# Kernel tuning notes

Hardware: AMD Instinct MI355X
Metric: run time of the kernel (lower is better)

## Reference

```python
import jax, jax.numpy as jnp
import numpy as np

H = 1024        # hidden_size
M = 1024        # memory_size
NH = 16         # num_heads
DH = H // NH    # head_dim
CR = 4          # compression_ratio
B, S = 4, 2048


def _lin(x, W, b):
    return x @ W + b


def setup_inputs() -> dict:
    key = jax.random.key(0)
    ks = iter(jax.random.split(key, 32))
    p = lambda *shape: jax.random.normal(next(ks), shape, dtype=jnp.float32) * 0.02
    inp = {
        'hidden_states': jax.random.normal(next(ks), (B, S, H), dtype=jnp.float32),
        'memory_bank': jax.random.normal(next(ks), (B, M, H), dtype=jnp.float32),
        'memory_mask': jnp.ones((B, M), dtype=bool),
        'write_pointer': 700,
        # compressor: Linear(H*CR -> H), SiLU, Linear(H -> H)
        'Wc1': p(H * CR, H), 'bc1': jnp.zeros((H,), jnp.float32),
        'Wc2': p(H, H), 'bc2': jnp.zeros((H,), jnp.float32),
        # attention projections
        'Wq': p(H, H), 'bq': jnp.zeros((H,), jnp.float32),
        'Wk': p(H, H), 'bk': jnp.zeros((H,), jnp.float32),
        'Wv': p(H, H), 'bv': jnp.zeros((H,), jnp.float32),
        'Wo': p(H, H), 'bo': jnp.zeros((H,), jnp.float32),
        # write gate: Linear(H -> H//2), SiLU, Linear(H//2 -> 1), Sigmoid
        'Wwg1': p(H, H // 2), 'bwg1': jnp.zeros((H // 2,), jnp.float32),
        'Wwg2': p(H // 2, 1), 'bwg2': jnp.zeros((1,), jnp.float32),
        # read gate: Linear(2H -> H//2), SiLU, Linear(H//2 -> 1), Sigmoid
        'Wrg1': p(2 * H, H // 2), 'brg1': jnp.zeros((H // 2,), jnp.float32),
        'Wrg2': p(H // 2, 1), 'brg2': jnp.zeros((1,), jnp.float32),
        # LayerNorm
        'ln_g': jnp.ones((H,), jnp.float32), 'ln_b': jnp.zeros((H,), jnp.float32),
    }
    return inp


def _forward(hidden_states, memory_bank, memory_mask, write_pointer,
             Wc1, bc1, Wc2, bc2, Wq, bq, Wk, bk, Wv, bv, Wo, bo,
             Wwg1, bwg1, Wwg2, bwg2, Wrg1, brg1, Wrg2, brg2, ln_g, ln_b):
    # ---- memory attention ----
    q = _lin(hidden_states, Wq, bq).reshape(B, S, NH, DH)
    k = _lin(memory_bank, Wk, bk).reshape(B, M, NH, DH)
    v = _lin(memory_bank, Wv, bv).reshape(B, M, NH, DH)
    scale = DH ** -0.5
    scores = jnp.einsum('bqhd,bkhd->bhqk', q, k) * scale
    scores = jnp.where(memory_mask[:, None, None, :], scores, -jnp.inf)
    probs = jnp.nan_to_num(jax.nn.softmax(scores, axis=-1), nan=0.0)
    retrieved = jnp.einsum('bhqk,bkhd->bqhd', probs, v).reshape(B, S, H)
    retrieved = _lin(retrieved, Wo, bo)

    # ---- read gate + residual + layernorm ----
    gate_in = jnp.concatenate([hidden_states, retrieved], axis=-1)
    rg = jax.nn.sigmoid(_lin(jax.nn.silu(_lin(gate_in, Wrg1, brg1)), Wrg2, brg2))
    out = hidden_states + rg * retrieved
    mu = jnp.mean(out, axis=-1, keepdims=True)
    var = jnp.var(out, axis=-1, keepdims=True)
    out = (out - mu) * jax.lax.rsqrt(var + 1e-5) * ln_g + ln_b

    # ---- write to memory ----
    wg = jax.nn.sigmoid(_lin(jax.nn.silu(_lin(hidden_states, Wwg1, bwg1)), Wwg2, bwg2))  # [B,S,1]
    L = S // CR  # S divisible by CR -> no padding needed (pad path is a no-op)
    compressed = _lin(jax.nn.silu(_lin(hidden_states.reshape(B, L, CR * H), Wc1, bc1)), Wc2, bc2)
    wg = wg.reshape(B, L, CR, 1).mean(axis=2)
    gated = compressed * wg  # [B,L,H]

    idx = (write_pointer + jnp.arange(L)) % M  # circular-buffer indices (unique since L <= M)
    new_bank = memory_bank.at[:, idx].set(gated)
    new_mask = memory_mask.at[:, idx].set(True)
    new_ptr = (write_pointer + L) % M
    return out, new_bank, new_mask, new_ptr


def reference(hidden_states, memory_bank, memory_mask, write_pointer,
              Wc1, bc1, Wc2, bc2, Wq, bq, Wk, bk, Wv, bv, Wo, bo,
              Wwg1, bwg1, Wwg2, bwg2, Wrg1, brg1, Wrg2, brg2, ln_g, ln_b):
    return _forward(hidden_states, memory_bank, memory_mask, write_pointer,
                    Wc1, bc1, Wc2, bc2, Wq, bq, Wk, bk, Wv, bv, Wo, bo,
                    Wwg1, bwg1, Wwg2, bwg2, Wrg1, brg1, Wrg2, brg2, ln_g, ln_b)
```

## Files before the change

### kernel.cpp

```cpp
#include <hip/hip_runtime.h>
#include <hip/hip_bf16.h>

#define Bb 4
#define Ss 2048
#define Hh 1024
#define Mm 1024
#define NHh 16
#define DHh 64
#define CRr 4
#define Ll (Ss / CRr)

typedef __attribute__((ext_vector_type(8))) short short8;
typedef __attribute__((ext_vector_type(4))) float f32x4;
typedef __attribute__((ext_vector_type(16))) float f32x16;

typedef __attribute__((address_space(1))) const unsigned int g_u32;
typedef __attribute__((address_space(3))) unsigned int l_u32;

__device__ inline void gload_lds16(const void* g, void* l) {
    __builtin_amdgcn_global_load_lds((g_u32*)g, (l_u32*)l, 16, 0, 0);
}

__device__ inline unsigned short f2bf(float x) {
    unsigned int u = __builtin_bit_cast(unsigned int, x);
    unsigned int r = u + 0x7FFFu + ((u >> 16) & 1u);
    return (unsigned short)(r >> 16);
}
__device__ inline float bf2f(unsigned short u) {
    return __builtin_bit_cast(float, (unsigned int)u << 16);
}
__device__ inline unsigned int cvtpk_bf16(float lo, float hi2) {
    unsigned int r;
    asm("v_cvt_pk_bf16_f32 %0, %1, %2" : "=v"(r) : "v"(lo), "v"(hi2));
    return r;
}
__device__ inline f32x16 zero16() {
    f32x16 v;
    #pragma unroll
    for (int i = 0; i < 16; ++i) v[i] = 0.0f;
    return v;
}
__device__ inline short8 lds_frag(const unsigned short* base, int row, int slot) {
    return *(const short8*)((const char*)base + row * 128 + ((slot ^ (row & 7)) << 4));
}

__global__ __launch_bounds__(256) void cast_bf16_kernel(
    const float* __restrict__ in, unsigned short* __restrict__ out, int n8)
{
    const int i = blockIdx.x * 256 + threadIdx.x;
    if (i >= n8) return;
    const float4* p = reinterpret_cast<const float4*>(in) + (size_t)i * 2;
    float4 a = p[0], b = p[1];
    uint4 o;
    o.x = (unsigned)f2bf(a.x) | ((unsigned)f2bf(a.y) << 16);
    o.y = (unsigned)f2bf(a.z) | ((unsigned)f2bf(a.w) << 16);
    o.z = (unsigned)f2bf(b.x) | ((unsigned)f2bf(b.y) << 16);
    o.w = (unsigned)f2bf(b.z) | ((unsigned)f2bf(b.w) << 16);
    *reinterpret_cast<uint4*>(out + (size_t)i * 8) = o;
}

__global__ __launch_bounds__(256) void transpose_cast_kernel(
    const float* __restrict__ W, unsigned short* __restrict__ Wt, int K, int N)
{
    __shared__ float tile[32][33];
    const int k0 = blockIdx.y * 32, n0 = blockIdx.x * 32;
    const int tx = threadIdx.x & 31, ty = threadIdx.x >> 5;
    #pragma unroll
    for (int r = 0; r < 32; r += 8)
        tile[r + ty][tx] = W[(size_t)(k0 + r + ty) * N + n0 + tx];
    __syncthreads();
    #pragma unroll
    for (int r = 0; r < 32; r += 8)
        Wt[(size_t)(n0 + r + ty) * K + k0 + tx] = f2bf(tile[tx][r + ty]);
}

__global__ __launch_bounds__(256) void gemm_bf16_kernel(
    const unsigned short* __restrict__ A1, const unsigned short* __restrict__ A2,
    int K1, const unsigned short* __restrict__ Wt, const float* __restrict__ bias,
    float* __restrict__ Cf, unsigned short* __restrict__ Cb,
    unsigned short* __restrict__ CbT,
    int Mdim, int Ndim, int Kdim, int act)
{
    __shared__ __align__(16) unsigned short As[128 * 64];
    __shared__ __align__(16) unsigned short Bs[128 * 64];

    const int t = threadIdx.x;
    const int l = t & 63;
    const int w = t >> 6;
    const int bm = blockIdx.y * 128;
    const int bn = blockIdx.x * 128;
    const int m_off = (w >> 1) * 64;
    const int n_off = (w & 1) * 64;
    const int K2 = Kdim - K1;

    f32x4 acc[4][4];
    const f32x4 z = {0.f, 0.f, 0.f, 0.f};
    #pragma unroll
    for (int i = 0; i < 4; ++i)
        #pragma unroll
        for (int j = 0; j < 4; ++j) acc[i][j] = z;

    for (int kt = 0; kt < Kdim; kt += 64) {
        __syncthreads();
        const unsigned short* Ap; int rsA, kl;
        if (kt < K1) { Ap = A1; rsA = K1; kl = kt; }
        else         { Ap = A2; rsA = K2; kl = kt - K1; }
        #pragma unroll
        for (int i = 0; i < 4; ++i) {
            const int c = i * 256 + t;
            const int row = c >> 3;
            const int p = (c & 7) ^ (row & 7);
            gload_lds16(Ap + (size_t)(bm + row) * rsA + kl + p * 8,
                        (char*)As + c * 16);
            gload_lds16(Wt + (size_t)(bn + row) * Kdim + kt + p * 8,
                        (char*)Bs + c * 16);
        }
        __syncthreads();
        #pragma unroll
        for (int kk = 0; kk < 2; ++kk) {
            short8 af[4], bfr[4];
            #pragma unroll
            for (int i = 0; i < 4; ++i) {
                af[i]  = lds_frag(As, m_off + i * 16 + (l & 15), kk * 4 + (l >> 4));
                bfr[i] = lds_frag(Bs, n_off + i * 16 + (l & 15), kk * 4 + (l >> 4));
            }
            #pragma unroll
            for (int i = 0; i < 4; ++i)
                #pragma unroll
                for (int j = 0; j < 4; ++j)
                    acc[i][j] = __builtin_amdgcn_mfma_f32_16x16x32_bf16(
                        af[i], bfr[j], acc[i][j], 0, 0, 0);
        }
    }

    #pragma unroll
    for (int j = 0; j < 4; ++j) {
        const int col = bn + n_off + j * 16 + (l & 15);
        const float bj = bias[col];
        #pragma unroll
        for (int i = 0; i < 4; ++i) {
            if (CbT) {
                const int row0 = bm + m_off + i * 16 + (l >> 4) * 4;
                const int bidx = row0 >> 10, key = row0 & 1023;
                ushort4 pk4;
                float v0 = acc[i][j][0] + bj, v1 = acc[i][j][1] + bj;
                float v2 = acc[i][j][2] + bj, v3 = acc[i][j][3] + bj;
                pk4.x = f2bf(v0); pk4.y = f2bf(v1);
                pk4.z = f2bf(v2); pk4.w = f2bf(v3);
                *(ushort4*)(CbT + ((size_t)bidx << 20) + (size_t)col * 1024 + key) = pk4;
            } else {
                #pragma unroll
                for (int r = 0; r < 4; ++r) {
                    const int row = bm + m_off + i * 16 + (l >> 4) * 4 + r;
                    float v0 = acc[i][j][r] + bj;
                    if (act == 1) v0 = v0 / (1.0f + __expf(-v0));
                    if (Cf) Cf[(size_t)row * Ndim + col] = v0;
                    if (Cb) Cb[(size_t)row * Ndim + col] = f2bf(v0);
                }
            }
        }
    }
}

__global__ __launch_bounds__(256) void attn_mfma_kernel(
    const unsigned short* __restrict__ q, const unsigned short* __restrict__ k,
    const unsigned short* __restrict__ vt, const unsigned char* __restrict__ mask,
    unsigned short* __restrict__ out)
{
    const int qt = blockIdx.x, h = blockIdx.y, b = blockIdx.z;
    const int t = threadIdx.x, l = t & 63, w = t >> 6;
    const int lq = l & 31, hi = l >> 5;

    __shared__ __align__(16) unsigned short Ks[64 * 64];
    __shared__ __align__(16) unsigned short Vs[64 * 64];

    short8 qf[4];
    {
        const int qg = qt * 128 + w * 32 + lq;
        const unsigned short* qp = q + ((size_t)(b * Ss + qg)) * Hh + h * 64 + hi * 8;
        #pragma unroll
        for (int tt = 0; tt < 4; ++tt) qf[tt] = *(const short8*)(qp + tt * 16);
    }

    f32x16 oacc0 = zero16(), oacc1 = zero16();
    float m_run = -3.0e38f, l_run = 0.0f;

    for (int c = 0; c < Mm / 64; ++c) {
        const int kc = c * 64;
        __syncthreads();
        {
            const int c0 = t, c1 = t + 256;
            const int r0 = c0 >> 3, s0 = c0 & 7;
            const int r1 = c1 >> 3, s1 = c1 & 7;
            gload_lds16(k + ((size_t)(b * Mm + kc + r0)) * Hh + h * 64 + ((s0 ^ (r0 & 7)) * 8),
                        (char*)Ks + c0 * 16);
            gload_lds16(k + ((size_t)(b * Mm + kc + r1)) * Hh + h * 64 + ((s1 ^ (r1 & 7)) * 8),
                        (char*)Ks + c1 * 16);
            gload_lds16(vt + ((size_t)b << 20) + (size_t)(h * 64 + r0) * Mm + kc + ((s0 ^ (r0 & 7)) * 8),
                        (char*)Vs + c0 * 16);
            gload_lds16(vt + ((size_t)b << 20) + (size_t)(h * 64 + r1) * Mm + kc + ((s1 ^ (r1 & 7)) * 8),
                        (char*)Vs + c1 * 16);
        }
        __syncthreads();

        f32x16 st0 = zero16(), st1 = zero16();
        #pragma unroll
        for (int tt = 0; tt < 4; ++tt) {
            short8 k0 = lds_frag(Ks, lq,      2 * tt + hi);
            short8 k1 = lds_frag(Ks, 32 + lq, 2 * tt + hi);
            st0 = __builtin_amdgcn_mfma_f32_32x32x16_bf16(k0, qf[tt], st0, 0, 0, 0);
            st1 = __builtin_amdgcn_mfma_f32_32x32x16_bf16(k1, qf[tt], st1, 0, 0, 0);
        }

        float sv[32];
        #pragma unroll
        for (int kb = 0; kb < 2; ++kb) {
            const f32x16 stv = kb ? st1 : st0;
            #pragma unroll
            for (int g = 0; g < 4; ++g) {
                const unsigned int mu = *(const unsigned int*)
                    (mask + b * Mm + kc + kb * 32 + 8 * g + 4 * hi);
                #pragma unroll
                for (int j = 0; j < 4; ++j) {
                    const float s = stv[g * 4 + j] * 0.125f;
                    sv[kb * 16 + g * 4 + j] = ((mu >> (8 * j)) & 1) ? s : -3.0e38f;
                }
            }
        }

        float mx = sv[0];
        #pragma unroll
        for (int i = 1; i < 32; ++i) mx = fmaxf(mx, sv[i]);
        mx = fmaxf(mx, __shfl_xor(mx, 32));
        const float m_new = fmaxf(m_run, mx);
        const float fac = __expf(m_run - m_new);
        m_run = m_new;

        float psum = 0.0f;
        #pragma unroll
        for (int i = 0; i < 32; ++i) {
            const float pv = (sv[i] > -1.0e37f) ? __expf(sv[i] - m_new) : 0.0f;
            sv[i] = pv; psum += pv;
        }
        psum += __shfl_xor(psum, 32);
        l_run = l_run * fac + psum;

        #pragma unroll
        for (int i = 0; i < 16; ++i) { oacc0[i] *= fac; oacc1[i] *= fac; }

        short8 pf[4];
        #pragma unroll
        for (int kb = 0; kb < 2; ++kb) {
            #pragma unroll
            for (int gp = 0; gp < 2; ++gp) {
                const float* pp = &sv[kb * 16 + gp * 8];
                unsigned int u  = cvtpk_bf16(pp[0], pp[1]);
                unsigned int v2 = cvtpk_bf16(pp[2], pp[3]);
                unsigned int w2 = cvtpk_bf16(pp[4], pp[5]);
                unsigned int z2 = cvtpk_bf16(pp[6], pp[7]);
                unsigned int su = __shfl_xor(u, 32),  sv2 = __shfl_xor(v2, 32);
                unsigned int sw = __shfl_xor(w2, 32), sz  = __shfl_xor(z2, 32);
                const bool low = (hi == 0);
                union { unsigned int d[4]; short8 s; } fr;
                fr.d[0] = low ? u   : sw;
                fr.d[1] = low ? v2  : sz;
                fr.d[2] = low ? su  : w2;
                fr.d[3] = low ? sv2 : z2;
                pf[kb * 2 + gp] = fr.s;
            }
        }

        #pragma unroll
        for (int ks = 0; ks < 4; ++ks) {
            short8 v0 = lds_frag(Vs, lq,      2 * ks + hi);
            short8 v1 = lds_frag(Vs, 32 + lq, 2 * ks + hi);
            oacc0 = __builtin_amdgcn_mfma_f32_32x32x16_bf16(v0, pf[ks], oacc0, 0, 0, 0);
            oacc1 = __builtin_amdgcn_mfma_f32_32x32x16_bf16(v1, pf[ks], oacc1, 0, 0, 0);
        }
    }

    const float inv = (l_run > 0.0f) ? 1.0f / l_run : 0.0f;
    const int qg = qt * 128 + w * 32 + lq;
    unsigned short* op = out + ((size_t)(b * Ss + qg)) * Hh + h * 64;
    #pragma unroll
    for (int db = 0; db < 2; ++db) {
        const f32x16 oa = db ? oacc1 : oacc0;
        #pragma unroll
        for (int g = 0; g < 4; ++g) {
            const int d0 = db * 32 + 8 * g + 4 * hi;
            ushort4 pk4;
            pk4.x = f2bf(oa[g * 4 + 0] * inv);
            pk4.y = f2bf(oa[g * 4 + 1] * inv);
            pk4.z = f2bf(oa[g * 4 + 2] * inv);
            pk4.w = f2bf(oa[g * 4 + 3] * inv);
            *(ushort4*)(op + d0) = pk4;
        }
    }
}

__global__ __launch_bounds__(256) void gate2_kernel(
    const unsigned short* __restrict__ h, const float* __restrict__ w2,
    const float* __restrict__ b2, float* __restrict__ outg, int R)
{
    const int wid = threadIdx.x / 64;
    const int lane = threadIdx.x % 64;
    const int row = blockIdx.x * 4 + wid;
    if (row >= R) return;
    short8 hv = *(const short8*)(h + (size_t)row * 512 + lane * 8);
    float4 w0 = *(const float4*)(w2 + lane * 8);
    float4 w1 = *(const float4*)(w2 + lane * 8 + 4);
    float s = bf2f((unsigned short)hv[0]) * w0.x + bf2f((unsigned short)hv[1]) * w0.y +
              bf2f((unsigned short)hv[2]) * w0.z + bf2f((unsigned short)hv[3]) * w0.w +
              bf2f((unsigned short)hv[4]) * w1.x + bf2f((unsigned short)hv[5]) * w1.y +
              bf2f((unsigned short)hv[6]) * w1.z + bf2f((unsigned short)hv[7]) * w1.w;
    #pragma unroll
    for (int o = 1; o < 64; o <<= 1) s += __shfl_xor(s, o);
    if (lane == 0) outg[row] = 1.0f / (1.0f + __expf(-(s + b2[0])));
}

__global__ __launch_bounds__(256) void out_ln_kernel(
    const float* __restrict__ hs, const unsigned short* __restrict__ retr,
    const float* __restrict__ rg, const float* __restrict__ gam,
    const float* __restrict__ bet, float* __restrict__ out)
{
    const int row = blockIdx.x;
    const int t = threadIdx.x;
    const float r = rg[row];
    float x[4];
    float s = 0.0f, s2 = 0.0f;
    #pragma unroll
    for (int i = 0; i < 4; ++i) {
        const int col = t + i * 256;
        const float val = hs[(size_t)row * Hh + col] +
                          r * bf2f(retr[(size_t)row * Hh + col]);
        x[i] = val; s += val; s2 += val * val;
    }
    #pragma unroll
    for (int o = 1; o < 64; o <<= 1) { s += __shfl_xor(s, o); s2 += __shfl_xor(s2, o); }
    __shared__ float rs[4], rs2[4];
    const int wid = t / 64, lane = t % 64;
    if (lane == 0) { rs[wid] = s; rs2[wid] = s2; }
    __syncthreads();
    const float tot = rs[0] + rs[1] + rs[2] + rs[3];
    const float tot2 = rs2[0] + rs2[1] + rs2[2] + rs2[3];
    const float mu = tot * (1.0f / Hh);
    const float var = tot2 * (1.0f / Hh) - mu * mu;
    const float rstd = rsqrtf(var + 1e-5f);
    #pragma unroll
    for (int i = 0; i < 4; ++i) {
        const int col = t + i * 256;
        out[(size_t)row * Hh + col] = (x[i] - mu) * rstd * gam[col] + bet[col];
    }
}

__global__ void wgmean_kernel(const float* __restrict__ wg_row,
                              float* __restrict__ wg_L)
{
    const int i = blockIdx.x * 256 + threadIdx.x;
    if (i < Bb * Ll)
        wg_L[i] = 0.25f * (wg_row[4 * i] + wg_row[4 * i + 1] +
                           wg_row[4 * i + 2] + wg_row[4 * i + 3]);
}

__global__ __launch_bounds__(256) void scatter_kernel(
    const float* __restrict__ comp, const float* __restrict__ wgL,
    const int* __restrict__ wp_ptr, float* __restrict__ bank_out)
{
    const int row = blockIdx.x;
    const int b = row / Ll, lx = row % Ll;
    const int wp = *wp_ptr;
    const int m = (wp + lx) % Mm;
    const float g = wgL[row];
    const int col = threadIdx.x * 4;
    float4 cv = *reinterpret_cast<const float4*>(comp + (size_t)row * Hh + col);
    cv.x *= g; cv.y *= g; cv.z *= g; cv.w *= g;
    *reinterpret_cast<float4*>(bank_out + ((size_t)(b * Mm + m)) * Hh + col) = cv;
}

__global__ void maskptr_kernel(const unsigned char* __restrict__ mask,
                               const int* __restrict__ wp_ptr,
                               float* __restrict__ mask_out,
                               float* __restrict__ ptr_out)
{
    const int i = blockIdx.x * 256 + threadIdx.x;
    const int wp = *wp_ptr;
    if (i < Bb * Mm) {
        const int m = i % Mm;
        int rel = m - (wp % Mm);
        if (rel < 0) rel += Mm;
        mask_out[i] = (mask[i] != 0 || rel < Ll) ? 1.0f : 0.0f;
    }
    if (i == 0) ptr_out[0] = (float)((wp + Ll) % Mm);
}

extern "C" void kernel_launch(void* const* d_in, const int* in_sizes, int n_in,
                              void* d_out, int out_size, void* d_ws, size_t ws_size,
                              hipStream_t stream)
{
    const float* hs   = (const float*)d_in[0];
    const float* bank = (const float*)d_in[1];
    const unsigned char* mask = (const unsigned char*)d_in[2];
    const int*   wp   = (const int*)d_in[3];
    const float* Wc1 = (const float*)d_in[4];  const float* bc1 = (const float*)d_in[5];
    const float* Wc2 = (const float*)d_in[6];  const float* bc2 = (const float*)d_in[7];
    const float* Wq  = (const float*)d_in[8];  const float* bq  = (const float*)d_in[9];
    const float* Wk  = (const float*)d_in[10]; const float* bk  = (const float*)d_in[11];
    const float* Wv  = (const float*)d_in[12]; const float* bv  = (const float*)d_in[13];
    const float* Wo  = (const float*)d_in[14]; const float* bo  = (const float*)d_in[15];
    const float* Wwg1 = (const float*)d_in[16]; const float* bwg1 = (const float*)d_in[17];
    const float* Wwg2 = (const float*)d_in[18]; const float* bwg2 = (const float*)d_in[19];
    const float* Wrg1 = (const float*)d_in[20]; const float* brg1 = (const float*)d_in[21];
    const float* Wrg2 = (const float*)d_in[22]; const float* brg2 = (const float*)d_in[23];
    const float* ln_g = (const float*)d_in[24]; const float* ln_b = (const float*)d_in[25];

    float* out_main = (float*)d_out;
    float* out_bank = out_main + (size_t)Bb * Ss * Hh;
    float* out_mask = out_bank + (size_t)Bb * Mm * Hh;
    float* out_ptr  = out_mask + (size_t)Bb * Mm;

    char* W = (char*)d_ws;
    unsigned short* hs_bf  = (unsigned short*)(W + 0);
    unsigned short* attslt = (unsigned short*)(W + 16777216);
    unsigned short* big1   = (unsigned short*)(W + 33554432);
    unsigned short* wslot  = (unsigned short*)(W + 50331648);
    char*           big2   = W + 58720256;
    char*           reg3   = W + 75497472;

    unsigned short* att_bf  = attslt;
    unsigned short* q_bf    = big1;
    unsigned short* retr_bf = big1;
    unsigned short* k_bf    = (unsigned short*)(big2);
    unsigned short* vt_bf   = (unsigned short*)(big2 + 8388608);
    unsigned short* bank_bf = (unsigned short*)(reg3);
    unsigned short* rg_h    = (unsigned short*)big2;
    unsigned short* wg_h    = (unsigned short*)big2;
    float* rg     = (float*)(reg3);
    float* wg_row = (float*)(reg3 + 32768);
    float* wg_L   = (float*)(reg3 + 65536);
    unsigned short* comp_h = attslt;
    float* comp   = (float*)((char*)attslt + 4194304);

    const int R = Bb * Ss;

    cast_bf16_kernel<<<4096, 256, 0, stream>>>(hs, hs_bf, R * Hh / 8);
    cast_bf16_kernel<<<2048, 256, 0, stream>>>(bank, bank_bf, Bb * Mm * Hh / 8);

    transpose_cast_kernel<<<dim3(32, 32), 256, 0, stream>>>(Wq, wslot, Hh, Hh);
    gemm_bf16_kernel<<<dim3(8, 64), 256, 0, stream>>>(
        hs_bf, hs_bf, Hh, wslot, bq, nullptr, q_bf, nullptr, R, Hh, Hh, 0);
    transpose_cast_kernel<<<dim3(32, 32), 256, 0, stream>>>(Wk, wslot, Hh, Hh);
    gemm_bf16_kernel<<<dim3(8, 32), 256, 0, stream>>>(
        bank_bf, bank_bf, Hh, wslot, bk, nullptr, k_bf, nullptr, Bb * Mm, Hh, Hh, 0);
    transpose_cast_kernel<<<dim3(32, 32), 256, 0, stream>>>(Wv, wslot, Hh, Hh);
    gemm_bf16_kernel<<<dim3(8, 32), 256, 0, stream>>>(
        bank_bf, bank_bf, Hh, wslot, bv, nullptr, nullptr, vt_bf, Bb * Mm, Hh, Hh, 0);

    attn_mfma_kernel<<<dim3(Ss / 128, NHh, Bb), 256, 0, stream>>>(
        q_bf, k_bf, vt_bf, mask, att_bf);

    transpose_cast_kernel<<<dim3(32, 32), 256, 0, stream>>>(Wo, wslot, Hh, Hh);
    gemm_bf16_kernel<<<dim3(8, 64), 256, 0, stream>>>(
        att_bf, att_bf, Hh, wslot, bo, nullptr, retr_bf, nullptr, R, Hh, Hh, 0);

    transpose_cast_kernel<<<dim3(16, 64), 256, 0, stream>>>(Wrg1, wslot, 2 * Hh, 512);
    gemm_bf16_kernel<<<dim3(4, 64), 256, 0, stream>>>(
        hs_bf, retr_bf, Hh, wslot, brg1, nullptr, rg_h, nullptr, R, 512, 2 * Hh, 1);
    gate2_kernel<<<R / 4, 256, 0, stream>>>(rg_h, Wrg2, brg2, rg, R);

    out_ln_kernel<<<R, 256, 0, stream>>>(hs, retr_bf, rg, ln_g, ln_b, out_main);

    transpose_cast_kernel<<<dim3(16, 32), 256, 0, stream>>>(Wwg1, wslot, Hh, 512);
    gemm_bf16_kernel<<<dim3(4, 64), 256, 0, stream>>>(
        hs_bf, hs_bf, Hh, wslot, bwg1, nullptr, wg_h, nullptr, R, 512, Hh, 1);
    gate2_kernel<<<R / 4, 256, 0, stream>>>(wg_h, Wwg2, bwg2, wg_row, R);
    wgmean_kernel<<<(Bb * Ll + 255) / 256, 256, 0, stream>>>(wg_row, wg_L);

    transpose_cast_kernel<<<dim3(32, 128), 256, 0, stream>>>(Wc1, wslot, CRr * Hh, Hh);
    gemm_bf16_kernel<<<dim3(8, 16), 256, 0, stream>>>(
        hs_bf, hs_bf, CRr * Hh, wslot, bc1, nullptr, comp_h, nullptr, Bb * Ll, Hh, CRr * Hh, 1);
    transpose_cast_kernel<<<dim3(32, 32), 256, 0, stream>>>(Wc2, wslot, Hh, Hh);
    gemm_bf16_kernel<<<dim3(8, 16), 256, 0, stream>>>(
        comp_h, comp_h, Hh, wslot, bc2, comp, nullptr, nullptr, Bb * Ll, Hh, Hh, 0);

    hipMemcpyAsync(out_bank, bank, (size_t)Bb * Mm * Hh * sizeof(float),
                   hipMemcpyDeviceToDevice, stream);
    scatter_kernel<<<Bb * Ll, 256, 0, stream>>>(comp, wg_L, wp, out_bank);

    maskptr_kernel<<<(Bb * Mm + 255) / 256, 256, 0, stream>>>(
        mask, wp, out_mask, out_ptr);
}
```

Baseline: 606.9 us.

## Fuse weight casts, merge GEMMs, and fold gates and scatter into epilogues

All weight transposes and casts now run in one launch, and the two input casts run in another. Q and write-gate-1 share a single GEMM, and K and V share another. The attention softmax uses an exp2 path with a precomputed mask bias and lazily rescales only when the running max grows by more than a threshold. The read-gate second stage is folded into the LayerNorm kernel. The compressor's final GEMM writes gated rows directly into the output bank, so the separate memcpy and scatter go away, and a fix-up kernel copies only the rows that were not written. Output buffers are reused as scratch, and workgroup swizzling is added to the GEMM. Together this cuts launch count and memory traffic, but the aliasing and the lazy-rescale threshold add correctness risk.

```diff
diff --git a/kernel.cpp b/kernel.cpp
--- a/kernel.cpp
+++ b/kernel.cpp
@@ -10,6 +10,8 @@
 #define CRr 4
 #define Ll (Ss / CRr)
 
+#define SC2 0.18033688f
+
 typedef __attribute__((ext_vector_type(8))) short short8;
 typedef __attribute__((ext_vector_type(4))) float f32x4;
 typedef __attribute__((ext_vector_type(16))) float f32x16;
@@ -44,42 +46,77 @@
     return *(const short8*)((const char*)base + row * 128 + ((slot ^ (row & 7)) << 4));
 }
 
-__global__ __launch_bounds__(256) void cast_bf16_kernel(
-    const float* __restrict__ in, unsigned short* __restrict__ out, int n8)
-{
-    const int i = blockIdx.x * 256 + threadIdx.x;
-    if (i >= n8) return;
-    const float4* p = reinterpret_cast<const float4*>(in) + (size_t)i * 2;
+#define N8_HS  (Bb * Ss * Hh / 8)
+#define N8_BK  (Bb * Mm * Hh / 8)
+__global__ __launch_bounds__(256) void cast2_kernel(
+    const float* __restrict__ hs, const float* __restrict__ bank,
+    unsigned short* __restrict__ hs_bf, unsigned short* __restrict__ bank_bf)
+{
+    int i = blockIdx.x * 256 + threadIdx.x;
+    const float* src; unsigned short* dst;
+    if (i < N8_HS) { src = hs; dst = hs_bf; }
+    else           { src = bank; dst = bank_bf; i -= N8_HS; if (i >= N8_BK) return; }
+    const float4* p = reinterpret_cast<const float4*>(src) + (size_t)i * 2;
     float4 a = p[0], b = p[1];
     uint4 o;
     o.x = (unsigned)f2bf(a.x) | ((unsigned)f2bf(a.y) << 16);
     o.y = (unsigned)f2bf(a.z) | ((unsigned)f2bf(a.w) << 16);
     o.z = (unsigned)f2bf(b.x) | ((unsigned)f2bf(b.y) << 16);
     o.w = (unsigned)f2bf(b.z) | ((unsigned)f2bf(b.w) << 16);
-    *reinterpret_cast<uint4*>(out + (size_t)i * 8) = o;
-}
-
-__global__ __launch_bounds__(256) void transpose_cast_kernel(
-    const float* __restrict__ W, unsigned short* __restrict__ Wt, int K, int N)
-{
+    *reinterpret_cast<uint4*>(dst + (size_t)i * 8) = o;
+}
+
+__global__ __launch_bounds__(256) void transpose_all_kernel(
+    const float* __restrict__ Wq, const float* __restrict__ Wwg1,
+    const float* __restrict__ Wk, const float* __restrict__ Wv,
+    const float* __restrict__ Wo, const float* __restrict__ Wrg1,
+    const float* __restrict__ Wc1, const float* __restrict__ Wc2,
+    unsigned short* wtQW, unsigned short* wtKV, unsigned short* wtO,
+    unsigned short* wtRG, unsigned short* wtC1, unsigned short* wtC2)
+{
+    int bid = blockIdx.x;
+    const float* src; unsigned short* dst; int K, N;
+    if (bid < 1024)      { src = Wq;   dst = wtQW;              K = 1024; N = 1024; }
+    else if (bid < 1536) { src = Wwg1; dst = wtQW + 1048576;    K = 1024; N = 512;  bid -= 1024; }
+    else if (bid < 2560) { src = Wk;   dst = wtKV;              K = 1024; N = 1024; bid -= 1536; }
+    else if (bid < 3584) { src = Wv;   dst = wtKV + 1048576;    K = 1024; N = 1024; bid -= 2560; }
+    else if (bid < 4608) { src = Wo;   dst = wtO;               K = 1024; N = 1024; bid -= 3584; }
+    else if (bid < 5632) { src = Wrg1; dst = wtRG;              K = 2048; N = 512;  bid -= 4608; }
+    else if (bid < 9728) { src = Wc1;  dst = wtC1;              K = 4096; N = 1024; bid -= 5632; }
+    else                 { src = Wc2;  dst = wtC2;              K = 1024; N = 1024; bid -= 9728; }
+    const int ntx = N >> 5;
+    const int k0 = (bid / ntx) * 32, n0 = (bid % ntx) * 32;
+
     __shared__ float tile[32][33];
-    const int k0 = blockIdx.y * 32, n0 = blockIdx.x * 32;
     const int tx = threadIdx.x & 31, ty = threadIdx.x >> 5;
     #pragma unroll
     for (int r = 0; r < 32; r += 8)
-        tile[r + ty][tx] = W[(size_t)(k0 + r + ty) * N + n0 + tx];
+        tile[r + ty][tx] = src[(size_t)(k0 + r + ty) * N + n0 + tx];
     __syncthreads();
     #pragma unroll
     for (int r = 0; r < 32; r += 8)
-        Wt[(size_t)(n0 + r + ty) * K + k0 + tx] = f2bf(tile[tx][r + ty]);
-}
+        dst[(size_t)(n0 + r + ty) * K + k0 + tx] = f2bf(tile[tx][r + ty]);
+}
+
+__global__ void maskbias_kernel(const unsigned char* __restrict__ mask,
+                                float* __restrict__ bias_arr)
+{
+    const int i = blockIdx.x * 256 + threadIdx.x;
+    if (i < Bb * Mm) bias_arr[i] = mask[i] ? 0.0f : -1.0e30f;
+}
+
+#define GM_BF16  0
+#define GM_BF16S 1
+#define GM_BF16T 2
+#define GM_F32G  3
 
 __global__ __launch_bounds__(256) void gemm_bf16_kernel(
     const unsigned short* __restrict__ A1, const unsigned short* __restrict__ A2,
-    int K1, const unsigned short* __restrict__ Wt, const float* __restrict__ bias,
-    float* __restrict__ Cf, unsigned short* __restrict__ Cb,
-    unsigned short* __restrict__ CbT,
-    int Mdim, int Ndim, int Kdim, int act)
+    int K1, const unsigned short* __restrict__ Wt,
+    const float* __restrict__ bias1, const float* __restrict__ bias2, int N1,
+    void* out1, void* out2, int mode1, int mode2,
+    int Mdim, int Ntot, int Kdim,
+    const int* __restrict__ wp_ptr, const float* __restrict__ wg_row)
 {
     __shared__ __align__(16) unsigned short As[128 * 64];
     __shared__ __align__(16) unsigned short Bs[128 * 64];
@@ -87,8 +124,14 @@
     const int t = threadIdx.x;
     const int l = t & 63;
     const int w = t >> 6;
-    const int bm = blockIdx.y * 128;
-    const int bn = blockIdx.x * 128;
+
+    const int nx = gridDim.x;
+    const int nwg = nx * gridDim.y;
+    const int bid0 = blockIdx.y * nx + blockIdx.x;
+    const int swz = (nwg & 7) ? bid0 : ((bid0 & 7) * (nwg >> 3) + (bid0 >> 3));
+    const int bm = (swz / nx) * 128;
+    const int bn = (swz % nx) * 128;
+
     const int m_off = (w >> 1) * 64;
     const int n_off = (w & 1) * 64;
     const int K2 = Kdim - K1;
@@ -133,38 +176,70 @@
         }
     }
 
+    float gg[16]; int wpv = 0;
+    if (mode1 == GM_F32G) {
+        wpv = *wp_ptr;
+        #pragma unroll
+        for (int i = 0; i < 4; ++i)
+            #pragma unroll
+            for (int r = 0; r < 4; ++r) {
+                const int row = bm + m_off + i * 16 + (l >> 4) * 4 + r;
+                gg[i * 4 + r] = 0.25f * (wg_row[4 * row] + wg_row[4 * row + 1] +
+                                         wg_row[4 * row + 2] + wg_row[4 * row + 3]);
+            }
+    }
+
     #pragma unroll
     for (int j = 0; j < 4; ++j) {
         const int col = bn + n_off + j * 16 + (l & 15);
-        const float bj = bias[col];
-        #pragma unroll
-        for (int i = 0; i < 4; ++i) {
-            if (CbT) {
+        const bool sec = (col >= N1);
+        const int cl = sec ? col - N1 : col;
+        const int mode = sec ? mode2 : mode1;
+        const float bj = sec ? bias2[cl] : bias1[cl];
+        const int nd = sec ? (Ntot - N1) : N1;
+        if (mode == GM_BF16T) {
+            unsigned short* ob = (unsigned short*)out2;
+            #pragma unroll
+            for (int i = 0; i < 4; ++i) {
                 const int row0 = bm + m_off + i * 16 + (l >> 4) * 4;
                 const int bidx = row0 >> 10, key = row0 & 1023;
                 ushort4 pk4;
-                float v0 = acc[i][j][0] + bj, v1 = acc[i][j][1] + bj;
-                float v2 = acc[i][j][2] + bj, v3 = acc[i][j][3] + bj;
-                pk4.x = f2bf(v0); pk4.y = f2bf(v1);
-                pk4.z = f2bf(v2); pk4.w = f2bf(v3);
-                *(ushort4*)(CbT + ((size_t)bidx << 20) + (size_t)col * 1024 + key) = pk4;
-            } else {
+                pk4.x = f2bf(acc[i][j][0] + bj);
+                pk4.y = f2bf(acc[i][j][1] + bj);
+                pk4.z = f2bf(acc[i][j][2] + bj);
+                pk4.w = f2bf(acc[i][j][3] + bj);
+                *(ushort4*)(ob + ((size_t)bidx << 20) + (size_t)cl * 1024 + key) = pk4;
+            }
+        } else if (mode == GM_F32G) {
+            float* ob = (float*)out1;
+            #pragma unroll
+            for (int i = 0; i < 4; ++i)
+                #pragma unroll
+                for (int r = 0; r < 4; ++r) {
+                    const int row = bm + m_off + i * 16 + (l >> 4) * 4 + r;
+                    const int bb = row >> 9, lx = row & 511;
+                    const int m = (wpv + lx) & 1023;
+                    ob[((size_t)(bb * 1024 + m)) * 1024 + col] =
+                        (acc[i][j][r] + bj) * gg[i * 4 + r];
+                }
+        } else {
+            unsigned short* ob = (unsigned short*)(sec ? out2 : out1);
+            #pragma unroll
+            for (int i = 0; i < 4; ++i)
                 #pragma unroll
                 for (int r = 0; r < 4; ++r) {
                     const int row = bm + m_off + i * 16 + (l >> 4) * 4 + r;
                     float v0 = acc[i][j][r] + bj;
-                    if (act == 1) v0 = v0 / (1.0f + __expf(-v0));
-                    if (Cf) Cf[(size_t)row * Ndim + col] = v0;
-                    if (Cb) Cb[(size_t)row * Ndim + col] = f2bf(v0);
+                    if (mode == GM_BF16S) v0 = v0 / (1.0f + __expf(-v0));
+                    ob[(size_t)row * nd + cl] = f2bf(v0);
                 }
-            }
         }
     }
 }
 
 __global__ __launch_bounds__(256) void attn_mfma_kernel(
     const unsigned short* __restrict__ q, const unsigned short* __restrict__ k,
-    const unsigned short* __restrict__ vt, const unsigned char* __restrict__ mask,
+    const unsigned short* __restrict__ vt, const float* __restrict__ bias_arr,
     unsigned short* __restrict__ out)
 {
     const int qt = blockIdx.x, h = blockIdx.y, b = blockIdx.z;
@@ -183,7 +258,7 @@
     }
 
     f32x16 oacc0 = zero16(), oacc1 = zero16();
-    float m_run = -3.0e38f, l_run = 0.0f;
+    float m_run = -1.0e38f, l_run = 0.0f;
 
     for (int c = 0; c < Mm / 64; ++c) {
         const int kc = c * 64;
@@ -218,35 +293,38 @@
             const f32x16 stv = kb ? st1 : st0;
             #pragma unroll
             for (int g = 0; g < 4; ++g) {
-                const unsigned int mu = *(const unsigned int*)
-                    (mask + b * Mm + kc + kb * 32 + 8 * g + 4 * hi);
-                #pragma unroll
-                for (int j = 0; j < 4; ++j) {
-                    const float s = stv[g * 4 + j] * 0.125f;
-                    sv[kb * 16 + g * 4 + j] = ((mu >> (8 * j)) & 1) ? s : -3.0e38f;
-                }
+                const float4 bf4 = *(const float4*)
+                    (bias_arr + b * Mm + kc + kb * 32 + 8 * g + 4 * hi);
+                sv[kb * 16 + g * 4 + 0] = fmaf(stv[g * 4 + 0], SC2, bf4.x);
+                sv[kb * 16 + g * 4 + 1] = fmaf(stv[g * 4 + 1], SC2, bf4.y);
+                sv[kb * 16 + g * 4 + 2] = fmaf(stv[g * 4 + 2], SC2, bf4.z);
+                sv[kb * 16 + g * 4 + 3] = fmaf(stv[g * 4 + 3], SC2, bf4.w);
             }
         }
 
-        float mx = sv[0];
-        #pragma unroll
-        for (int i = 1; i < 32; ++i) mx = fmaxf(mx, sv[i]);
+        float mx = fmaxf(sv[0], fmaxf(sv[1], sv[2]));
+        #pragma unroll
+        for (int i = 3; i < 31; i += 2) mx = fmaxf(mx, fmaxf(sv[i], sv[i + 1]));
+        mx = fmaxf(mx, sv[31]);
         mx = fmaxf(mx, __shfl_xor(mx, 32));
-        const float m_new = fmaxf(m_run, mx);
-        const float fac = __expf(m_run - m_new);
-        m_run = m_new;
+
+        if (!__all(mx <= m_run + 10.0f)) {
+            const float m_new = fmaxf(m_run, mx);
+            const float fac = exp2f(m_run - m_new);
+            m_run = m_new;
+            l_run *= fac;
+            #pragma unroll
+            for (int i = 0; i < 16; ++i) { oacc0[i] *= fac; oacc1[i] *= fac; }
+        }
 
         float psum = 0.0f;
         #pragma unroll
         for (int i = 0; i < 32; ++i) {
-            const float pv = (sv[i] > -1.0e37f) ? __expf(sv[i] - m_new) : 0.0f;
+            const float pv = exp2f(sv[i] - m_run);
             sv[i] = pv; psum += pv;
         }
         psum += __shfl_xor(psum, 32);
-        l_run = l_run * fac + psum;
-
-        #pragma unroll
-        for (int i = 0; i < 16; ++i) { oacc0[i] *= fac; oacc1[i] *= fac; }
+        l_run += psum;
 
         short8 pf[4];
         #pragma unroll
@@ -320,12 +398,25 @@
 
 __global__ __launch_bounds__(256) void out_ln_kernel(
     const float* __restrict__ hs, const unsigned short* __restrict__ retr,
-    const float* __restrict__ rg, const float* __restrict__ gam,
+    const unsigned short* __restrict__ rg_h, const float* __restrict__ Wrg2,
+    const float* __restrict__ brg2, const float* __restrict__ gam,
     const float* __restrict__ bet, float* __restrict__ out)
 {
     const int row = blockIdx.x;
     const int t = threadIdx.x;
-    const float r = rg[row];
+    const int wid = t >> 6, lane = t & 63;
+
+    const unsigned int hv = *(const unsigned int*)(rg_h + (size_t)row * 512 + t * 2);
+    const float2 wv = *(const float2*)(Wrg2 + t * 2);
+    float sd = bf2f((unsigned short)(hv & 0xffffu)) * wv.x +
+               bf2f((unsigned short)(hv >> 16)) * wv.y;
+    #pragma unroll
+    for (int o = 1; o < 64; o <<= 1) sd += __shfl_xor(sd, o);
+    __shared__ float rsd[4];
+    if (lane == 0) rsd[wid] = sd;
+    __syncthreads();
+    const float r = 1.0f / (1.0f + __expf(-(rsd[0] + rsd[1] + rsd[2] + rsd[3] + brg2[0])));
+
     float x[4];
     float s = 0.0f, s2 = 0.0f;
     #pragma unroll
@@ -338,7 +429,6 @@
     #pragma unroll
     for (int o = 1; o < 64; o <<= 1) { s += __shfl_xor(s, o); s2 += __shfl_xor(s2, o); }
     __shared__ float rs[4], rs2[4];
-    const int wid = t / 64, lane = t % 64;
     if (lane == 0) { rs[wid] = s; rs2[wid] = s2; }
     __syncthreads();
     const float tot = rs[0] + rs[1] + rs[2] + rs[3];
@@ -353,44 +443,24 @@
     }
 }
 
-__global__ void wgmean_kernel(const float* __restrict__ wg_row,
-                              float* __restrict__ wg_L)
-{
-    const int i = blockIdx.x * 256 + threadIdx.x;
-    if (i < Bb * Ll)
-        wg_L[i] = 0.25f * (wg_row[4 * i] + wg_row[4 * i + 1] +
-                           wg_row[4 * i + 2] + wg_row[4 * i + 3]);
-}
-
-__global__ __launch_bounds__(256) void scatter_kernel(
-    const float* __restrict__ comp, const float* __restrict__ wgL,
-    const int* __restrict__ wp_ptr, float* __restrict__ bank_out)
+__global__ __launch_bounds__(256) void bankfix_kernel(
+    const float* __restrict__ bank, const unsigned char* __restrict__ mask,
+    const int* __restrict__ wp_ptr, float* __restrict__ out_bank,
+    float* __restrict__ out_mask, float* __restrict__ out_ptr)
 {
     const int row = blockIdx.x;
-    const int b = row / Ll, lx = row % Ll;
     const int wp = *wp_ptr;
-    const int m = (wp + lx) % Mm;
-    const float g = wgL[row];
-    const int col = threadIdx.x * 4;
-    float4 cv = *reinterpret_cast<const float4*>(comp + (size_t)row * Hh + col);
-    cv.x *= g; cv.y *= g; cv.z *= g; cv.w *= g;
-    *reinterpret_cast<float4*>(bank_out + ((size_t)(b * Mm + m)) * Hh + col) = cv;
-}
-
-__global__ void maskptr_kernel(const unsigned char* __restrict__ mask,
-                               const int* __restrict__ wp_ptr,
-                               float* __restrict__ mask_out,
-                               float* __restrict__ ptr_out)
-{
-    const int i = blockIdx.x * 256 + threadIdx.x;
-    const int wp = *wp_ptr;
-    if (i < Bb * Mm) {
-        const int m = i % Mm;
-        int rel = m - (wp % Mm);
-        if (rel < 0) rel += Mm;
-        mask_out[i] = (mask[i] != 0 || rel < Ll) ? 1.0f : 0.0f;
-    }
-    if (i == 0) ptr_out[0] = (float)((wp + Ll) % Mm);
+    const int m = row & 1023;
+    int rel = m - (wp & 1023);
+    if (rel < 0) rel += Mm;
+    const bool written = rel < Ll;
+    if (!written) {
+        const int col = threadIdx.x * 4;
+        *(float4*)(out_bank + (size_t)row * Hh + col) =
+            *(const float4*)(bank + (size_t)row * Hh + col);
+    }
+    if (threadIdx.x == 0) out_mask[row] = (mask[row] != 0 || written) ? 1.0f : 0.0f;
+    if (row == 0 && threadIdx.x == 0) out_ptr[0] = (float)((wp + Ll) % Mm);
 }
 
 extern "C" void kernel_launch(void* const* d_in, const int* in_sizes, int n_in,
@@ -418,74 +488,68 @@
     float* out_mask = out_bank + (size_t)Bb * Mm * Hh;
     float* out_ptr  = out_mask + (size_t)Bb * Mm;
 
+    unsigned short* q_bf   = (unsigned short*)out_main;
+    unsigned short* att_bf = (unsigned short*)out_main + 8388608;
+    unsigned short* wtQW = (unsigned short*)out_bank;
+    unsigned short* wtO  = (unsigned short*)out_bank + 1572864;
+    unsigned short* wtRG = (unsigned short*)out_bank + 2621440;
+    unsigned short* wtC1 = (unsigned short*)out_bank + 3670016;
+
     char* W = (char*)d_ws;
-    unsigned short* hs_bf  = (unsigned short*)(W + 0);
-    unsigned short* attslt = (unsigned short*)(W + 16777216);
-    unsigned short* big1   = (unsigned short*)(W + 33554432);
-    unsigned short* wslot  = (unsigned short*)(W + 50331648);
-    char*           big2   = W + 58720256;
-    char*           reg3   = W + 75497472;
-
-    unsigned short* att_bf  = attslt;
-    unsigned short* q_bf    = big1;
-    unsigned short* retr_bf = big1;
-    unsigned short* k_bf    = (unsigned short*)(big2);
-    unsigned short* vt_bf   = (unsigned short*)(big2 + 8388608);
-    unsigned short* bank_bf = (unsigned short*)(reg3);
-    unsigned short* rg_h    = (unsigned short*)big2;
-    unsigned short* wg_h    = (unsigned short*)big2;
-    float* rg     = (float*)(reg3);
-    float* wg_row = (float*)(reg3 + 32768);
-    float* wg_L   = (float*)(reg3 + 65536);
-    unsigned short* comp_h = attslt;
-    float* comp   = (float*)((char*)attslt + 4194304);
-
-    const int R = Bb * Ss;
-
-    cast_bf16_kernel<<<4096, 256, 0, stream>>>(hs, hs_bf, R * Hh / 8);
-    cast_bf16_kernel<<<2048, 256, 0, stream>>>(bank, bank_bf, Bb * Mm * Hh / 8);
-
-    transpose_cast_kernel<<<dim3(32, 32), 256, 0, stream>>>(Wq, wslot, Hh, Hh);
+    unsigned short* hs_bf   = (unsigned short*)(W + 0);
+    unsigned short* bank_bf = (unsigned short*)(W + 16777216);
+    unsigned short* rg_h    = (unsigned short*)(W + 16777216);
+    unsigned short* retr_bf = (unsigned short*)(W + 25165824);
+    unsigned short* k_bf    = (unsigned short*)(W + 41943040);
+    unsigned short* vt_bf   = (unsigned short*)(W + 50331648);
+    unsigned short* comp_h  = (unsigned short*)(W + 50331648);
+    unsigned short* wg_h    = (unsigned short*)(W + 58720256);
+    unsigned short* wtC2    = (unsigned short*)(W + 67108864);
+    unsigned short* wtKV    = (unsigned short*)(W + 69206016);
+    float* wg_row   = (float*)(W + 73400320);
+    float* bias_arr = (float*)(W + 73433088);
+
+    cast2_kernel<<<(N8_HS + N8_BK + 255) / 256, 256, 0, stream>>>(
+        hs, bank, hs_bf, bank_bf);
+
+    transpose_all_kernel<<<10752, 256, 0, stream>>>(
+        Wq, Wwg1, Wk, Wv, Wo, Wrg1, Wc1, Wc2,
+        wtQW, wtKV, wtO, wtRG, wtC1, wtC2);
+
+    maskbias_kernel<<<16, 256, 0, stream>>>(mask, bias_arr);
+
+    gemm_bf16_kernel<<<dim3(12, 64), 256, 0, stream>>>(
+        hs_bf, hs_bf, Hh, wtQW, bq, bwg1, 1024,
+        q_bf, wg_h, GM_BF16, GM_BF16S, Bb * Ss, 1536, Hh, nullptr, nullptr);
+
+    gemm_bf16_kernel<<<dim3(16, 32), 256, 0, stream>>>(
+        bank_bf, bank_bf, Hh, wtKV, bk, bv, 1024,
+        k_bf, vt_bf, GM_BF16, GM_BF16T, Bb * Mm, 2048, Hh, nullptr, nullptr);
+
+    attn_mfma_kernel<<<dim3(Ss / 128, NHh, Bb), 256, 0, stream>>>(
+        q_bf, k_bf, vt_bf, bias_arr, att_bf);
+
     gemm_bf16_kernel<<<dim3(8, 64), 256, 0, stream>>>(
-        hs_bf, hs_bf, Hh, wslot, bq, nullptr, q_bf, nullptr, R, Hh, Hh, 0);
-    transpose_cast_kernel<<<dim3(32, 32), 256, 0, stream>>>(Wk, wslot, Hh, Hh);
-    gemm_bf16_kernel<<<dim3(8, 32), 256, 0, stream>>>(
-        bank_bf, bank_bf, Hh, wslot, bk, nullptr, k_bf, nullptr, Bb * Mm, Hh, Hh, 0);
-    transpose_cast_kernel<<<dim3(32, 32), 256, 0, stream>>>(Wv, wslot, Hh, Hh);
-    gemm_bf16_kernel<<<dim3(8, 32), 256, 0, stream>>>(
-        bank_bf, bank_bf, Hh, wslot, bv, nullptr, nullptr, vt_bf, Bb * Mm, Hh, Hh, 0);
-
-    attn_mfma_kernel<<<dim3(Ss / 128, NHh, Bb), 256, 0, stream>>>(
-        q_bf, k_bf, vt_bf, mask, att_bf);
-
-    transpose_cast_kernel<<<dim3(32, 32), 256, 0, stream>>>(Wo, wslot, Hh, Hh);
-    gemm_bf16_kernel<<<dim3(8, 64), 256, 0, stream>>>(
-        att_bf, att_bf, Hh, wslot, bo, nullptr, retr_bf, nullptr, R, Hh, Hh, 0);
-
-    transpose_cast_kernel<<<dim3(16, 64), 256, 0, stream>>>(Wrg1, wslot, 2 * Hh, 512);
+        att_bf, att_bf, Hh, wtO, bo, bo, 1024,
+        retr_bf, nullptr, GM_BF16, GM_BF16, Bb * Ss, 1024, Hh, nullptr, nullptr);
+
     gemm_bf16_kernel<<<dim3(4, 64), 256, 0, stream>>>(
-        hs_bf, retr_bf, Hh, wslot, brg1, nullptr, rg_h, nullptr, R, 512, 2 * Hh, 1);
-    gate2_kernel<<<R / 4, 256, 0, stream>>>(rg_h, Wrg2, brg2, rg, R);
-
-    out_ln_kernel<<<R, 256, 0, stream>>>(hs, retr_bf, rg, ln_g, ln_b, out_main);
-
-    transpose_cast_kernel<<<dim3(16, 32), 256, 0, stream>>>(Wwg1, wslot, Hh, 512);
-    gemm_bf16_kernel<<<dim3(4, 64), 256, 0, stream>>>(
-        hs_bf, hs_bf, Hh, wslot, bwg1, nullptr, wg_h, nullptr, R, 512, Hh, 1);
-    gate2_kernel<<<R / 4, 256, 0, stream>>>(wg_h, Wwg2, bwg2, wg_row, R);
-    wgmean_kernel<<<(Bb * Ll + 255) / 256, 256, 0, stream>>>(wg_row, wg_L);
-
-    transpose_cast_kernel<<<dim3(32, 128), 256, 0, stream>>>(Wc1, wslot, CRr * Hh, Hh);
+        hs_bf, retr_bf, Hh, wtRG, brg1, brg1, 512,
+        rg_h, nullptr, GM_BF16S, GM_BF16S, Bb * Ss, 512, 2 * Hh, nullptr, nullptr);
+
+    gate2_kernel<<<Bb * Ss / 4, 256, 0, stream>>>(wg_h, Wwg2, bwg2, wg_row, Bb * Ss);
+
+    out_ln_kernel<<<Bb * Ss, 256, 0, stream>>>(
+        hs, retr_bf, rg_h, Wrg2, brg2, ln_g, ln_b, out_main);
+
     gemm_bf16_kernel<<<dim3(8, 16), 256, 0, stream>>>(
-        hs_bf, hs_bf, CRr * Hh, wslot, bc1, nullptr, comp_h, nullptr, Bb * Ll, Hh, CRr * Hh, 1);
-    transpose_cast_kernel<<<dim3(32, 32), 256, 0, stream>>>(Wc2, wslot, Hh, Hh);
+        hs_bf, hs_bf, CRr * Hh, wtC1, bc1, bc1, 1024,
+        comp_h, nullptr, GM_BF16S, GM_BF16S, Bb * Ll, 1024, CRr * Hh, nullptr, nullptr);
+
     gemm_bf16_kernel<<<dim3(8, 16), 256, 0, stream>>>(
-        comp_h, comp_h, Hh, wslot, bc2, comp, nullptr, nullptr, Bb * Ll, Hh, Hh, 0);
-
-    hipMemcpyAsync(out_bank, bank, (size_t)Bb * Mm * Hh * sizeof(float),
-                   hipMemcpyDeviceToDevice, stream);
-    scatter_kernel<<<Bb * Ll, 256, 0, stream>>>(comp, wg_L, wp, out_bank);
-
-    maskptr_kernel<<<(Bb * Mm + 255) / 256, 256, 0, stream>>>(
-        mask, wp, out_mask, out_ptr);
-}
+        comp_h, comp_h, Hh, wtC2, bc2, bc2, 1024,
+        out_bank, nullptr, GM_F32G, GM_F32G, Bb * Ll, 1024, Hh, wp, wg_row);
+
+    bankfix_kernel<<<Bb * Mm, 256, 0, stream>>>(
+        bank, mask, wp, out_bank, out_mask, out_ptr);
+}
```

Measured after the change: 530.4 us. -12.6%, faster.
